# Kernel optimization log

Hardware: AMD Instinct MI355X
Metric: run time of the kernel (lower is better)

Reference implementation:

```python
import jax, jax.numpy as jnp
import numpy as np

EPS = 1e-5
LORA_DIM = 64
LORA_SCALE = LORA_DIM ** (-0.5)
GRAD_SCALE = 0.5  # infeat_grad_scale (bp_to_unet=True path)


def _ln(x, g=None, b=None):
    mu = jnp.mean(x, axis=-1, keepdims=True)
    var = jnp.mean((x - mu) ** 2, axis=-1, keepdims=True)
    y = (x - mu) * jax.lax.rsqrt(var + EPS)
    if g is not None:
        y = y * g + b
    return y


def _grad_scale(t, s=GRAD_SCALE):
    # identity in forward, scales gradient by s in backward
    return t * s + jax.lax.stop_gradient(t) * (1.0 - s)


def setup_inputs() -> dict:
    key = jax.random.key(0)
    ks = jax.random.split(key, 8)
    B, C, H, W = 32, 1280, 32, 32
    TD, LD = 768, LORA_DIM
    inp = {}
    inp["layer_infeat"] = jax.random.normal(ks[0], (B, C, H, W), jnp.float32)
    inp["layer_inquery"] = jax.random.normal(ks[1], (B, H * W, C), jnp.float32)
    inp["token_q_emb"] = jax.random.normal(ks[2], (TD,), jnp.float32)
    # learned params
    inp["to_q_w"] = jax.random.normal(ks[3], (C, TD), jnp.float32) * (TD ** -0.5)
    inp["ln_x_g"] = jnp.ones((C,), jnp.float32)
    inp["ln_x_b"] = jnp.zeros((C,), jnp.float32)
    inp["ln_k_g"] = jnp.ones((C,), jnp.float32)
    inp["ln_k_b"] = jnp.zeros((C,), jnp.float32)
    inp["ln_q_g"] = jnp.ones((TD,), jnp.float32)
    inp["ln_q_b"] = jnp.zeros((TD,), jnp.float32)
    inp["lora_q_w"] = jax.random.normal(ks[4], (LD, C), jnp.float32) * (C ** -0.5)
    inp["lora_k_w"] = jax.random.normal(ks[5], (LD, C), jnp.float32) * (C ** -0.5)
    inp["mask"] = jax.random.randint(ks[6], (B, 1, H, W), 0, 2).astype(jnp.float32)
    return inp


def reference(layer_infeat, layer_inquery, token_q_emb, to_q_w,
              ln_x_g, ln_x_b, ln_k_g, ln_k_b, ln_q_g, ln_q_b,
              lora_q_w, lora_k_w, mask):
    B, C, H, W = layer_infeat.shape
    # flatten(2).permute(0,2,1): [B,C,H,W] -> [B, HW, C]
    x = _grad_scale(layer_infeat).reshape(B, C, H * W).transpose(0, 2, 1)
    k_in = _grad_scale(layer_inquery)
    # q = to_q(ln_q(token_q_emb[None])) -> [1, C], broadcast to [B, 1, C]
    q = _ln(token_q_emb[None, :], ln_q_g, ln_q_b) @ to_q_w.T
    q = jnp.broadcast_to(q[None], (B, 1, C))
    k = _ln(k_in, ln_k_g, ln_k_b)   # [B, HW, C]
    v = _ln(x, ln_x_g, ln_x_b)      # [B, HW, C]
    # LoRA score path (use_lora=True since lora_dim>0)
    lora_q = _ln(q) @ lora_q_w.T    # [B, 1, LD]
    lora_k = _ln(k) @ lora_k_w.T    # [B, HW, LD]
    sim = jnp.einsum('bid,bjd->bij', lora_q, lora_k) * LORA_SCALE  # [B,1,HW]
    # mask: nearest interpolation to (H,W) is identity (same size); flatten
    m = mask.reshape(B, 1, H * W) > 0
    sim = jnp.where(m, sim, -jnp.finfo(sim.dtype).max)
    attn = jax.nn.softmax(sim, axis=-1)
    fg = jnp.einsum('bij,bjd->bid', attn, v)            # [B, 1, C]
    bg = jnp.mean(v, axis=1, keepdims=True) - fg        # [B, 1, C]
    out = jnp.concatenate([fg, bg], axis=-1)            # [B, 1, 2C]
    return out[:, 0, :]                                  # [B, 2C]
```

## Files before the change

kernel.cpp:

```cpp
#include <hip/hip_runtime.h>
#include <math.h>

#define B_   32
#define CD   1280
#define HW_  1024
#define TD_  768
#define LD_  64
#define EPSF 1e-5f
#define LORA_SCALE_F 0.125f

__device__ __forceinline__ float wredSum(float a) {
#pragma unroll
  for (int o = 32; o; o >>= 1) a += __shfl_xor(a, o, 64);
  return a;
}
__device__ __forceinline__ void wred2(float& a, float& b) {
#pragma unroll
  for (int o = 32; o; o >>= 1) { a += __shfl_xor(a, o, 64); b += __shfl_xor(b, o, 64); }
}
__device__ __forceinline__ float blockSum(float v, float* red) {
  int t = threadIdx.x;
  red[t] = v; __syncthreads();
#pragma unroll
  for (int s = 128; s > 0; s >>= 1) { if (t < s) red[t] += red[t + s]; __syncthreads(); }
  float r = red[0]; __syncthreads();
  return r;
}
__device__ __forceinline__ float blockMax(float v, float* red) {
  int t = threadIdx.x;
  red[t] = v; __syncthreads();
#pragma unroll
  for (int s = 128; s > 0; s >>= 1) { if (t < s) red[t] = fmaxf(red[t], red[t + s]); __syncthreads(); }
  float r = red[0]; __syncthreads();
  return r;
}
__device__ __forceinline__ void blockSum2(float& a, float& b, float2* red) {
  int t = threadIdx.x;
  red[t] = make_float2(a, b); __syncthreads();
#pragma unroll
  for (int s = 128; s > 0; s >>= 1) {
    if (t < s) { red[t].x += red[t + s].x; red[t].y += red[t + s].y; }
    __syncthreads();
  }
  a = red[0].x; b = red[0].y; __syncthreads();
}

__global__ __launch_bounds__(256) void kA12(const float* __restrict__ tq,
                                            const float* __restrict__ lng,
                                            const float* __restrict__ lnb,
                                            const float* __restrict__ to_q_w,
                                            float* __restrict__ q_out) {
  __shared__ float lnq[TD_];
  __shared__ float2 red[256];
  int t = threadIdx.x;
  float s = 0.f, ss = 0.f, vals[3];
#pragma unroll
  for (int k = 0; k < 3; k++) { float v = tq[t + 256 * k]; vals[k] = v; s += v; ss += v * v; }
  blockSum2(s, ss, red);
  float mu = s * (1.f / TD_);
  float r = rsqrtf(ss * (1.f / TD_) - mu * mu + EPSF);
#pragma unroll
  for (int k = 0; k < 3; k++) { int i = t + 256 * k; lnq[i] = (vals[k] - mu) * r * lng[i] + lnb[i]; }
  __syncthreads();
  int c = blockIdx.x * 4 + (t >> 6);
  int lane = t & 63;
  const float4* w4 = (const float4*)(to_q_w + (size_t)c * TD_);
  const float4* l4 = (const float4*)lnq;
  float dot = 0.f;
#pragma unroll
  for (int i = 0; i < 3; i++) {
    int f = i * 64 + lane;
    float4 w = w4[f], l = l4[f];
    dot += w.x * l.x + w.y * l.y + w.z * l.z + w.w * l.w;
  }
  dot = wredSum(dot);
  if (lane == 0) q_out[c] = dot;
}

__global__ __launch_bounds__(256) void kA34(const float* __restrict__ q_in,
                                            const float* __restrict__ lora_q_w,
                                            float* __restrict__ lq_out) {
  __shared__ float qs[CD];
  __shared__ float2 red[256];
  int t = threadIdx.x;
  float s = 0.f, ss = 0.f, vals[5];
#pragma unroll
  for (int k = 0; k < 5; k++) { float v = q_in[t + 256 * k]; vals[k] = v; s += v; ss += v * v; }
  blockSum2(s, ss, red);
  float mu = s * (1.f / CD);
  float r = rsqrtf(ss * (1.f / CD) - mu * mu + EPSF);
#pragma unroll
  for (int k = 0; k < 5; k++) { int i = t + 256 * k; qs[i] = (vals[k] - mu) * r; }
  __syncthreads();
  int d = blockIdx.x * 4 + (t >> 6);
  int lane = t & 63;
  const float4* w4 = (const float4*)(lora_q_w + (size_t)d * CD);
  const float4* q4 = (const float4*)qs;
  float dot = 0.f;
#pragma unroll
  for (int i = 0; i < 5; i++) {
    int f = i * 64 + lane;
    float4 w = w4[f], qq = q4[f];
    dot += w.x * qq.x + w.y * qq.y + w.z * qq.z + w.w * qq.w;
  }
  dot = wredSum(dot);
  if (lane == 0) lq_out[d] = dot;
}

__global__ __launch_bounds__(256) void kA56(const float* __restrict__ lq,
                                            const float* __restrict__ lora_k_w,
                                            float* __restrict__ w_eff) {
  __shared__ float l[LD_];
  int t = threadIdx.x;
  if (t < LD_) l[t] = lq[t];
  __syncthreads();
  int c = blockIdx.x * 256 + t;
  float acc = 0.f;
#pragma unroll 8
  for (int d = 0; d < LD_; d++) acc += l[d] * lora_k_w[(size_t)d * CD + c];
  w_eff[c] = acc;
}

__global__ __launch_bounds__(256) void kB(const float* __restrict__ kin,
                                          const float* __restrict__ g,
                                          const float* __restrict__ bb,
                                          const float* __restrict__ w_eff,
                                          float* __restrict__ sim) {
  __shared__ float4 gs[CD / 4], bs[CD / 4], ws[CD / 4];
  __shared__ float red[256];
  int t = threadIdx.x;
  float wsum = 0.f;
  for (int k = t; k < CD / 4; k += 256) {
    float4 w = ((const float4*)w_eff)[k];
    ws[k] = w;
    gs[k] = ((const float4*)g)[k];
    bs[k] = ((const float4*)bb)[k];
    wsum += w.x + w.y + w.z + w.w;
  }
  float W0 = blockSum(wsum, red);
  int wid = t >> 6, lane = t & 63;
  int gw = blockIdx.x * 4 + wid;
  for (int row = gw; row < B_ * HW_; row += 8192) {
    const float4* x4 = (const float4*)(kin + (size_t)row * CD);
    float4 xv[5];
    float s = 0.f, ss = 0.f;
#pragma unroll
    for (int i = 0; i < 5; i++) {
      float4 v = x4[i * 64 + lane];
      xv[i] = v;
      s += v.x + v.y + v.z + v.w;
      ss += v.x * v.x + v.y * v.y + v.z * v.z + v.w * v.w;
    }
    wred2(s, ss);
    float mu1 = s * (1.f / CD);
    float r1 = rsqrtf(ss * (1.f / CD) - mu1 * mu1 + EPSF);
    float s2 = 0.f, ss2 = 0.f;
#pragma unroll
    for (int i = 0; i < 5; i++) {
      int f = i * 64 + lane;
      float4 G = gs[f], Bv = bs[f], v = xv[i], kk;
      kk.x = (v.x - mu1) * r1 * G.x + Bv.x;
      kk.y = (v.y - mu1) * r1 * G.y + Bv.y;
      kk.z = (v.z - mu1) * r1 * G.z + Bv.z;
      kk.w = (v.w - mu1) * r1 * G.w + Bv.w;
      xv[i] = kk;
      s2 += kk.x + kk.y + kk.z + kk.w;
      ss2 += kk.x * kk.x + kk.y * kk.y + kk.z * kk.z + kk.w * kk.w;
    }
    wred2(s2, ss2);
    float mu2 = s2 * (1.f / CD);
    float r2 = rsqrtf(ss2 * (1.f / CD) - mu2 * mu2 + EPSF);
    float dot = 0.f;
#pragma unroll
    for (int i = 0; i < 5; i++) {
      float4 w = ws[i * 64 + lane], kk = xv[i];
      dot += w.x * kk.x + w.y * kk.y + w.z * kk.z + w.w * kk.w;
    }
    dot = wredSum(dot);
    if (lane == 0) sim[row] = LORA_SCALE_F * r2 * (dot - mu2 * W0);
  }
}

__global__ __launch_bounds__(256) void kD1(const float* __restrict__ infeat,
                                           float* __restrict__ mu_out,
                                           float* __restrict__ r_out) {
  int tile = blockIdx.x & 15, b = blockIdx.x >> 4;
  int t = threadIdx.x;
  int jg = t & 15;
  int slice = t >> 4;
  int j0 = tile * 64 + jg * 4;
  const float* base = infeat + (size_t)b * CD * HW_ + j0;
  float4 s = make_float4(0, 0, 0, 0), q = make_float4(0, 0, 0, 0);
  int c0 = slice * 80;
#pragma unroll 4
  for (int c = c0; c < c0 + 80; c++) {
    float4 v = *(const float4*)(base + (size_t)c * HW_);
    s.x += v.x; s.y += v.y; s.z += v.z; s.w += v.w;
    q.x += v.x * v.x; q.y += v.y * v.y; q.z += v.z * v.z; q.w += v.w * v.w;
  }
  __shared__ float4 sArr[16][16], qArr[16][16];
  sArr[slice][jg] = s; qArr[slice][jg] = q;
  __syncthreads();
#pragma unroll
  for (int st = 8; st > 0; st >>= 1) {
    if (slice < st) {
      float4 a = sArr[slice][jg], b2 = sArr[slice + st][jg];
      a.x += b2.x; a.y += b2.y; a.z += b2.z; a.w += b2.w;
      sArr[slice][jg] = a;
      a = qArr[slice][jg]; b2 = qArr[slice + st][jg];
      a.x += b2.x; a.y += b2.y; a.z += b2.z; a.w += b2.w;
      qArr[slice][jg] = a;
    }
    __syncthreads();
  }
  if (slice == 0) {
    float4 S = sArr[0][jg], Q = qArr[0][jg], mu, r;
    mu.x = S.x * (1.f / CD); mu.y = S.y * (1.f / CD);
    mu.z = S.z * (1.f / CD); mu.w = S.w * (1.f / CD);
    r.x = rsqrtf(Q.x * (1.f / CD) - mu.x * mu.x + EPSF);
    r.y = rsqrtf(Q.y * (1.f / CD) - mu.y * mu.y + EPSF);
    r.z = rsqrtf(Q.z * (1.f / CD) - mu.z * mu.z + EPSF);
    r.w = rsqrtf(Q.w * (1.f / CD) - mu.w * mu.w + EPSF);
    int j = b * HW_ + j0;
    *(float4*)(mu_out + j) = mu;
    *(float4*)(r_out + j) = r;
  }
}

__global__ __launch_bounds__(256) void kC(const float* __restrict__ sim,
                                          const float* __restrict__ mask,
                                          const float* __restrict__ mu,
                                          const float* __restrict__ r,
                                          float* __restrict__ w1,
                                          float* __restrict__ w2,
                                          float* __restrict__ S1,
                                          float* __restrict__ S3) {
  __shared__ float red[256];
  __shared__ float2 red2[256];
  int b = blockIdx.x, t = threadIdx.x;
  float4 sv = ((const float4*)(sim + b * HW_))[t];
  float4 mv = ((const float4*)(mask + b * HW_))[t];
  float4 muv = ((const float4*)(mu + b * HW_))[t];
  float4 rv = ((const float4*)(r + b * HW_))[t];
  const float NEG = -3.4028235e38f;
  float se0 = mv.x > 0.f ? sv.x : NEG;
  float se1 = mv.y > 0.f ? sv.y : NEG;
  float se2 = mv.z > 0.f ? sv.z : NEG;
  float se3 = mv.w > 0.f ? sv.w : NEG;
  float m = fmaxf(fmaxf(se0, se1), fmaxf(se2, se3));
  float M = blockMax(m, red);
  float e0 = expf(se0 - M), e1 = expf(se1 - M), e2 = expf(se2 - M), e3 = expf(se3 - M);
  float Z = blockSum(e0 + e1 + e2 + e3, red);
  float inv = 1.f / Z;
  float a0 = e0 * inv, a1 = e1 * inv, a2 = e2 * inv, a3 = e3 * inv;
  float4 w1v = make_float4(a0 * rv.x, a1 * rv.y, a2 * rv.z, a3 * rv.w);
  float4 w2v = make_float4(rv.x * (1.f / HW_), rv.y * (1.f / HW_),
                           rv.z * (1.f / HW_), rv.w * (1.f / HW_));
  float s1 = w1v.x * muv.x + w1v.y * muv.y + w1v.z * muv.z + w1v.w * muv.w;
  float s3 = w2v.x * muv.x + w2v.y * muv.y + w2v.z * muv.z + w2v.w * muv.w;
  blockSum2(s1, s3, red2);
  ((float4*)(w1 + b * HW_))[t] = w1v;
  ((float4*)(w2 + b * HW_))[t] = w2v;
  if (t == 0) { S1[b] = s1; S3[b] = s3; }
}

__global__ __launch_bounds__(256) void kD2(const float* __restrict__ infeat,
                                           const float* __restrict__ w1,
                                           const float* __restrict__ w2,
                                           const float* __restrict__ S1,
                                           const float* __restrict__ S3,
                                           const float* __restrict__ g,
                                           const float* __restrict__ bb,
                                           float* __restrict__ out) {
  __shared__ float4 w1s[HW_ / 4], w2s[HW_ / 4];
  int t = threadIdx.x;
  int b = blockIdx.x / 40, tile = blockIdx.x % 40;
  w1s[t] = ((const float4*)(w1 + b * HW_))[t];
  w2s[t] = ((const float4*)(w2 + b * HW_))[t];
  __syncthreads();
  int wid = t >> 6, lane = t & 63;
  float s1 = S1[b], s3 = S3[b];
#pragma unroll
  for (int k = 0; k < 8; k++) {
    int c = tile * 32 + wid * 8 + k;
    const float4* x4 = (const float4*)(infeat + (size_t)b * CD * HW_ + (size_t)c * HW_);
    float d1 = 0.f, d2 = 0.f;
#pragma unroll
    for (int i = 0; i < 4; i++) {
      int f = i * 64 + lane;
      float4 x = x4[f], a = w1s[f], w = w2s[f];
      d1 += x.x * a.x + x.y * a.y + x.z * a.z + x.w * a.w;
      d2 += x.x * w.x + x.y * w.y + x.z * w.z + x.w * w.w;
    }
    wred2(d1, d2);
    if (lane == 0) {
      float gc = g[c], bc = bb[c];
      float fg = gc * (d1 - s1) + bc;
      float vm = gc * (d2 - s3) + bc;
      out[(size_t)b * (2 * CD) + c] = fg;
      out[(size_t)b * (2 * CD) + CD + c] = vm - fg;
    }
  }
}

extern "C" void kernel_launch(void* const* d_in, const int* in_sizes, int n_in,
                              void* d_out, int out_size, void* d_ws, size_t ws_size,
                              hipStream_t stream) {
  const float* infeat  = (const float*)d_in[0];
  const float* inquery = (const float*)d_in[1];
  const float* tq      = (const float*)d_in[2];
  const float* to_q_w  = (const float*)d_in[3];
  const float* ln_x_g  = (const float*)d_in[4];
  const float* ln_x_b  = (const float*)d_in[5];
  const float* ln_k_g  = (const float*)d_in[6];
  const float* ln_k_b  = (const float*)d_in[7];
  const float* ln_q_g  = (const float*)d_in[8];
  const float* ln_q_b  = (const float*)d_in[9];
  const float* lora_q_w = (const float*)d_in[10];
  const float* lora_k_w = (const float*)d_in[11];
  const float* mask    = (const float*)d_in[12];
  float* out = (float*)d_out;

  float* ws = (float*)d_ws;
  float* q_ws    = ws;
  float* lq_ws   = ws + 1280;
  float* weff_ws = ws + 1344;
  float* sim_ws  = ws + 2624;
  float* mu_ws   = ws + 35392;
  float* r_ws    = ws + 68160;
  float* w1_ws   = ws + 100928;
  float* w2_ws   = ws + 133696;
  float* S1_ws   = ws + 166464;
  float* S3_ws   = ws + 166496;

  kA12<<<320, 256, 0, stream>>>(tq, ln_q_g, ln_q_b, to_q_w, q_ws);
  kA34<<<16, 256, 0, stream>>>(q_ws, lora_q_w, lq_ws);
  kA56<<<5, 256, 0, stream>>>(lq_ws, lora_k_w, weff_ws);
  kB<<<2048, 256, 0, stream>>>(inquery, ln_k_g, ln_k_b, weff_ws, sim_ws);
  kD1<<<512, 256, 0, stream>>>(infeat, mu_ws, r_ws);
  kC<<<32, 256, 0, stream>>>(sim_ws, mask, mu_ws, r_ws, w1_ws, w2_ws, S1_ws, S3_ws);
  kD2<<<1280, 256, 0, stream>>>(infeat, w1_ws, w2_ws, S1_ws, S3_ws, ln_x_g, ln_x_b, out);
}
```

Baseline: 405.6 us.

## Fuse kernels, compute LN-of-LN scores via moment algebra, split infeat stats

Merges the query projection with the infeat channel-statistics pass into one launch, and folds the LoRA q/k weight prep into a single-block prep kernel. The prep kernel emits per-channel coefficients and global scalars so the key-row kernel computes the double layernorm and score from one pass of moment sums, without materialising normalised values. The infeat stats pass is split into four channel quarters for more blocks, and the softmax/weight kernel is fused into the final reduction, which now recomputes mu/r and softmax in every tile block. This cuts launches and per-row work at the cost of redundant softmax work, extra shuffles and a single-block serial prep step. The one-pass variance expansion may also lose some numerical precision.

```diff
diff --git a/kernel.cpp b/kernel.cpp
--- a/kernel.cpp
+++ b/kernel.cpp
@@ -8,6 +8,7 @@
 #define LD_  64
 #define EPSF 1e-5f
 #define LORA_SCALE_F 0.125f
+#define NROWS (B_ * HW_)
 
 __device__ __forceinline__ float wredSum(float a) {
 #pragma unroll
@@ -45,241 +46,276 @@
   a = red[0].x; b = red[0].y; __syncthreads();
 }
 
-__global__ __launch_bounds__(256) void kA12(const float* __restrict__ tq,
+__global__ __launch_bounds__(256) void kAD1(const float* __restrict__ tq,
                                             const float* __restrict__ lng,
                                             const float* __restrict__ lnb,
                                             const float* __restrict__ to_q_w,
-                                            float* __restrict__ q_out) {
-  __shared__ float lnq[TD_];
-  __shared__ float2 red[256];
-  int t = threadIdx.x;
-  float s = 0.f, ss = 0.f, vals[3];
-#pragma unroll
-  for (int k = 0; k < 3; k++) { float v = tq[t + 256 * k]; vals[k] = v; s += v; ss += v * v; }
-  blockSum2(s, ss, red);
-  float mu = s * (1.f / TD_);
-  float r = rsqrtf(ss * (1.f / TD_) - mu * mu + EPSF);
-#pragma unroll
-  for (int k = 0; k < 3; k++) { int i = t + 256 * k; lnq[i] = (vals[k] - mu) * r * lng[i] + lnb[i]; }
-  __syncthreads();
-  int c = blockIdx.x * 4 + (t >> 6);
-  int lane = t & 63;
-  const float4* w4 = (const float4*)(to_q_w + (size_t)c * TD_);
-  const float4* l4 = (const float4*)lnq;
-  float dot = 0.f;
-#pragma unroll
-  for (int i = 0; i < 3; i++) {
-    int f = i * 64 + lane;
-    float4 w = w4[f], l = l4[f];
-    dot += w.x * l.x + w.y * l.y + w.z * l.z + w.w * l.w;
-  }
-  dot = wredSum(dot);
-  if (lane == 0) q_out[c] = dot;
-}
-
-__global__ __launch_bounds__(256) void kA34(const float* __restrict__ q_in,
-                                            const float* __restrict__ lora_q_w,
-                                            float* __restrict__ lq_out) {
-  __shared__ float qs[CD];
-  __shared__ float2 red[256];
-  int t = threadIdx.x;
-  float s = 0.f, ss = 0.f, vals[5];
-#pragma unroll
-  for (int k = 0; k < 5; k++) { float v = q_in[t + 256 * k]; vals[k] = v; s += v; ss += v * v; }
-  blockSum2(s, ss, red);
-  float mu = s * (1.f / CD);
-  float r = rsqrtf(ss * (1.f / CD) - mu * mu + EPSF);
-#pragma unroll
-  for (int k = 0; k < 5; k++) { int i = t + 256 * k; qs[i] = (vals[k] - mu) * r; }
-  __syncthreads();
-  int d = blockIdx.x * 4 + (t >> 6);
-  int lane = t & 63;
-  const float4* w4 = (const float4*)(lora_q_w + (size_t)d * CD);
-  const float4* q4 = (const float4*)qs;
-  float dot = 0.f;
+                                            const float* __restrict__ infeat,
+                                            float* __restrict__ q_out,
+                                            float* __restrict__ Spart,
+                                            float* __restrict__ Qpart) {
+  __shared__ float smem[2048];
+  int t = threadIdx.x;
+  if (blockIdx.x < 320) {
+    float* lnq = smem;
+    float2* red = (float2*)(smem + 768);
+    float s = 0.f, ss = 0.f, vals[3];
+#pragma unroll
+    for (int k = 0; k < 3; k++) { float v = tq[t + 256 * k]; vals[k] = v; s += v; ss += v * v; }
+    blockSum2(s, ss, red);
+    float mu = s * (1.f / TD_);
+    float r = rsqrtf(ss * (1.f / TD_) - mu * mu + EPSF);
+#pragma unroll
+    for (int k = 0; k < 3; k++) { int i = t + 256 * k; lnq[i] = (vals[k] - mu) * r * lng[i] + lnb[i]; }
+    __syncthreads();
+    int c = blockIdx.x * 4 + (t >> 6);
+    int lane = t & 63;
+    const float4* w4 = (const float4*)(to_q_w + (size_t)c * TD_);
+    const float4* l4 = (const float4*)lnq;
+    float dot = 0.f;
+#pragma unroll
+    for (int i = 0; i < 3; i++) {
+      int f = i * 64 + lane;
+      float4 w = w4[f], l = l4[f];
+      dot += w.x * l.x + w.y * l.y + w.z * l.z + w.w * l.w;
+    }
+    dot = wredSum(dot);
+    if (lane == 0) q_out[c] = dot;
+  } else {
+    int idx = blockIdx.x - 320;
+    int b = idx >> 6;
+    int rr = idx & 63;
+    int tile = rr >> 2;
+    int qtr = rr & 3;
+    int jg = t & 15;
+    int slice = t >> 4;
+    int j0 = tile * 64 + jg * 4;
+    const float* base = infeat + (size_t)b * CD * HW_ + j0;
+    int c0 = qtr * 320 + slice * 20;
+    float4 s = make_float4(0, 0, 0, 0), q = make_float4(0, 0, 0, 0);
+#pragma unroll
+    for (int c = c0; c < c0 + 20; c++) {
+      float4 v = *(const float4*)(base + (size_t)c * HW_);
+      s.x += v.x; s.y += v.y; s.z += v.z; s.w += v.w;
+      q.x += v.x * v.x; q.y += v.y * v.y; q.z += v.z * v.z; q.w += v.w * v.w;
+    }
+    float4* sArr = (float4*)smem;
+    float4* qArr = (float4*)(smem + 1024);
+    sArr[slice * 16 + jg] = s; qArr[slice * 16 + jg] = q;
+    __syncthreads();
+#pragma unroll
+    for (int st = 8; st > 0; st >>= 1) {
+      if (slice < st) {
+        float4 a = sArr[slice * 16 + jg], b2 = sArr[(slice + st) * 16 + jg];
+        a.x += b2.x; a.y += b2.y; a.z += b2.z; a.w += b2.w;
+        sArr[slice * 16 + jg] = a;
+        a = qArr[slice * 16 + jg]; b2 = qArr[(slice + st) * 16 + jg];
+        a.x += b2.x; a.y += b2.y; a.z += b2.z; a.w += b2.w;
+        qArr[slice * 16 + jg] = a;
+      }
+      __syncthreads();
+    }
+    if (slice == 0) {
+      size_t o = ((size_t)(b * 4 + qtr) << 10) + j0;
+      *(float4*)(Spart + o) = sArr[jg];
+      *(float4*)(Qpart + o) = qArr[jg];
+    }
+  }
+}
+
+__global__ __launch_bounds__(1024) void kPrep(const float* __restrict__ q_in,
+                                              const float* __restrict__ lora_q_w,
+                                              const float* __restrict__ lora_k_w,
+                                              const float* __restrict__ kg,
+                                              const float* __restrict__ kb,
+                                              float4* __restrict__ coeff,
+                                              float* __restrict__ scalars) {
+  __shared__ float qn[CD];
+  __shared__ float lqs[LD_];
+  __shared__ float4 red4[1024];
+  int t = threadIdx.x;
+  float v0 = q_in[t];
+  float v1 = (t < CD - 1024) ? q_in[1024 + t] : 0.f;
+  red4[t] = make_float4(v0 + v1, v0 * v0 + v1 * v1, 0.f, 0.f);
+  __syncthreads();
+#pragma unroll
+  for (int st = 512; st > 0; st >>= 1) {
+    if (t < st) { red4[t].x += red4[t + st].x; red4[t].y += red4[t + st].y; }
+    __syncthreads();
+  }
+  float mu = red4[0].x * (1.f / CD);
+  float r = rsqrtf(red4[0].y * (1.f / CD) - mu * mu + EPSF);
+  __syncthreads();
+  qn[t] = (v0 - mu) * r;
+  if (t < CD - 1024) qn[1024 + t] = (v1 - mu) * r;
+  __syncthreads();
+  int w = t >> 6, lane = t & 63;
+  int d0 = w * 4;
+  const float4* qn4 = (const float4*)qn;
+  float dacc[4] = {0.f, 0.f, 0.f, 0.f};
 #pragma unroll
   for (int i = 0; i < 5; i++) {
     int f = i * 64 + lane;
-    float4 w = w4[f], qq = q4[f];
-    dot += w.x * qq.x + w.y * qq.y + w.z * qq.z + w.w * qq.w;
-  }
-  dot = wredSum(dot);
-  if (lane == 0) lq_out[d] = dot;
-}
-
-__global__ __launch_bounds__(256) void kA56(const float* __restrict__ lq,
-                                            const float* __restrict__ lora_k_w,
-                                            float* __restrict__ w_eff) {
-  __shared__ float l[LD_];
-  int t = threadIdx.x;
-  if (t < LD_) l[t] = lq[t];
-  __syncthreads();
-  int c = blockIdx.x * 256 + t;
-  float acc = 0.f;
-#pragma unroll 8
-  for (int d = 0; d < LD_; d++) acc += l[d] * lora_k_w[(size_t)d * CD + c];
-  w_eff[c] = acc;
+    float4 qv = qn4[f];
+#pragma unroll
+    for (int dd = 0; dd < 4; dd++) {
+      float4 wv = *(const float4*)(lora_q_w + (size_t)(d0 + dd) * CD + 4 * f);
+      dacc[dd] += wv.x * qv.x + wv.y * qv.y + wv.z * qv.z + wv.w * qv.w;
+    }
+  }
+#pragma unroll
+  for (int o = 32; o; o >>= 1) {
+#pragma unroll
+    for (int dd = 0; dd < 4; dd++) dacc[dd] += __shfl_xor(dacc[dd], o, 64);
+  }
+  if (lane == 0) {
+#pragma unroll
+    for (int dd = 0; dd < 4; dd++) lqs[d0 + dd] = dacc[dd];
+  }
+  __syncthreads();
+  float4 pA = make_float4(0, 0, 0, 0);
+  float4 pB = make_float4(0, 0, 0, 0);
+#pragma unroll
+  for (int pass = 0; pass < 2; pass++) {
+    int c = (pass == 0) ? t : 1024 + t;
+    if (pass == 0 || t < CD - 1024) {
+      float acc = 0.f;
+#pragma unroll 16
+      for (int d = 0; d < LD_; d++) acc += lqs[d] * lora_k_w[(size_t)d * CD + c];
+      float g = kg[c], b = kb[c], wv = acc;
+      coeff[c] = make_float4(g * g, g * b, wv * g, g);
+      pA.x += g; pA.y += g * g; pA.z += g * b; pA.w += b;
+      pB.x += b * b; pB.y += wv * g; pB.z += wv * b; pB.w += wv;
+    }
+  }
+  red4[t] = pA; __syncthreads();
+#pragma unroll
+  for (int st = 512; st > 0; st >>= 1) {
+    if (t < st) {
+      red4[t].x += red4[t + st].x; red4[t].y += red4[t + st].y;
+      red4[t].z += red4[t + st].z; red4[t].w += red4[t + st].w;
+    }
+    __syncthreads();
+  }
+  if (t == 0) {
+    scalars[0] = red4[0].x; scalars[1] = red4[0].y;
+    scalars[2] = red4[0].z; scalars[3] = red4[0].w;
+  }
+  __syncthreads();
+  red4[t] = pB; __syncthreads();
+#pragma unroll
+  for (int st = 512; st > 0; st >>= 1) {
+    if (t < st) {
+      red4[t].x += red4[t + st].x; red4[t].y += red4[t + st].y;
+      red4[t].z += red4[t + st].z; red4[t].w += red4[t + st].w;
+    }
+    __syncthreads();
+  }
+  if (t == 0) {
+    scalars[4] = red4[0].x; scalars[5] = red4[0].y;
+    scalars[6] = red4[0].z; scalars[7] = red4[0].w;
+  }
 }
 
 __global__ __launch_bounds__(256) void kB(const float* __restrict__ kin,
-                                          const float* __restrict__ g,
-                                          const float* __restrict__ bb,
-                                          const float* __restrict__ w_eff,
+                                          const float4* __restrict__ coeff,
+                                          const float* __restrict__ scalars,
                                           float* __restrict__ sim) {
-  __shared__ float4 gs[CD / 4], bs[CD / 4], ws[CD / 4];
-  __shared__ float red[256];
-  int t = threadIdx.x;
-  float wsum = 0.f;
-  for (int k = t; k < CD / 4; k += 256) {
-    float4 w = ((const float4*)w_eff)[k];
-    ws[k] = w;
-    gs[k] = ((const float4*)g)[k];
-    bs[k] = ((const float4*)bb)[k];
-    wsum += w.x + w.y + w.z + w.w;
-  }
-  float W0 = blockSum(wsum, red);
-  int wid = t >> 6, lane = t & 63;
-  int gw = blockIdx.x * 4 + wid;
-  for (int row = gw; row < B_ * HW_; row += 8192) {
+  int t = threadIdx.x, wid = t >> 6, lane = t & 63;
+  float4 cf[20];
+#pragma unroll
+  for (int i = 0; i < 5; i++) {
+    int f = i * 64 + lane;
+#pragma unroll
+    for (int k = 0; k < 4; k++) cf[i * 4 + k] = coeff[f * 4 + k];
+  }
+  float Sg = scalars[0], Sg2 = scalars[1], Sgb = scalars[2], Sb = scalars[3];
+  float Sb2 = scalars[4], Swg = scalars[5], Swb = scalars[6], W0 = scalars[7];
+  int row0 = blockIdx.x * 4 + wid;
+  for (int row = row0; row < NROWS; row += 8192) {
     const float4* x4 = (const float4*)(kin + (size_t)row * CD);
-    float4 xv[5];
-    float s = 0.f, ss = 0.f;
+    float sx = 0.f, sxx = 0.f, sA = 0.f, sB = 0.f, sC = 0.f, sD = 0.f, sE = 0.f;
 #pragma unroll
     for (int i = 0; i < 5; i++) {
       float4 v = x4[i * 64 + lane];
-      xv[i] = v;
-      s += v.x + v.y + v.z + v.w;
-      ss += v.x * v.x + v.y * v.y + v.z * v.z + v.w * v.w;
-    }
-    wred2(s, ss);
-    float mu1 = s * (1.f / CD);
-    float r1 = rsqrtf(ss * (1.f / CD) - mu1 * mu1 + EPSF);
-    float s2 = 0.f, ss2 = 0.f;
-#pragma unroll
-    for (int i = 0; i < 5; i++) {
-      int f = i * 64 + lane;
-      float4 G = gs[f], Bv = bs[f], v = xv[i], kk;
-      kk.x = (v.x - mu1) * r1 * G.x + Bv.x;
-      kk.y = (v.y - mu1) * r1 * G.y + Bv.y;
-      kk.z = (v.z - mu1) * r1 * G.z + Bv.z;
-      kk.w = (v.w - mu1) * r1 * G.w + Bv.w;
-      xv[i] = kk;
-      s2 += kk.x + kk.y + kk.z + kk.w;
-      ss2 += kk.x * kk.x + kk.y * kk.y + kk.z * kk.z + kk.w * kk.w;
-    }
-    wred2(s2, ss2);
-    float mu2 = s2 * (1.f / CD);
-    float r2 = rsqrtf(ss2 * (1.f / CD) - mu2 * mu2 + EPSF);
-    float dot = 0.f;
-#pragma unroll
-    for (int i = 0; i < 5; i++) {
-      float4 w = ws[i * 64 + lane], kk = xv[i];
-      dot += w.x * kk.x + w.y * kk.y + w.z * kk.z + w.w * kk.w;
-    }
-    dot = wredSum(dot);
-    if (lane == 0) sim[row] = LORA_SCALE_F * r2 * (dot - mu2 * W0);
-  }
-}
-
-__global__ __launch_bounds__(256) void kD1(const float* __restrict__ infeat,
-                                           float* __restrict__ mu_out,
-                                           float* __restrict__ r_out) {
-  int tile = blockIdx.x & 15, b = blockIdx.x >> 4;
-  int t = threadIdx.x;
-  int jg = t & 15;
-  int slice = t >> 4;
-  int j0 = tile * 64 + jg * 4;
-  const float* base = infeat + (size_t)b * CD * HW_ + j0;
-  float4 s = make_float4(0, 0, 0, 0), q = make_float4(0, 0, 0, 0);
-  int c0 = slice * 80;
-#pragma unroll 4
-  for (int c = c0; c < c0 + 80; c++) {
-    float4 v = *(const float4*)(base + (size_t)c * HW_);
-    s.x += v.x; s.y += v.y; s.z += v.z; s.w += v.w;
-    q.x += v.x * v.x; q.y += v.y * v.y; q.z += v.z * v.z; q.w += v.w * v.w;
-  }
-  __shared__ float4 sArr[16][16], qArr[16][16];
-  sArr[slice][jg] = s; qArr[slice][jg] = q;
-  __syncthreads();
-#pragma unroll
-  for (int st = 8; st > 0; st >>= 1) {
-    if (slice < st) {
-      float4 a = sArr[slice][jg], b2 = sArr[slice + st][jg];
-      a.x += b2.x; a.y += b2.y; a.z += b2.z; a.w += b2.w;
-      sArr[slice][jg] = a;
-      a = qArr[slice][jg]; b2 = qArr[slice + st][jg];
-      a.x += b2.x; a.y += b2.y; a.z += b2.z; a.w += b2.w;
-      qArr[slice][jg] = a;
-    }
-    __syncthreads();
-  }
-  if (slice == 0) {
-    float4 S = sArr[0][jg], Q = qArr[0][jg], mu, r;
-    mu.x = S.x * (1.f / CD); mu.y = S.y * (1.f / CD);
-    mu.z = S.z * (1.f / CD); mu.w = S.w * (1.f / CD);
-    r.x = rsqrtf(Q.x * (1.f / CD) - mu.x * mu.x + EPSF);
-    r.y = rsqrtf(Q.y * (1.f / CD) - mu.y * mu.y + EPSF);
-    r.z = rsqrtf(Q.z * (1.f / CD) - mu.z * mu.z + EPSF);
-    r.w = rsqrtf(Q.w * (1.f / CD) - mu.w * mu.w + EPSF);
-    int j = b * HW_ + j0;
-    *(float4*)(mu_out + j) = mu;
-    *(float4*)(r_out + j) = r;
-  }
-}
-
-__global__ __launch_bounds__(256) void kC(const float* __restrict__ sim,
-                                          const float* __restrict__ mask,
-                                          const float* __restrict__ mu,
-                                          const float* __restrict__ r,
-                                          float* __restrict__ w1,
-                                          float* __restrict__ w2,
-                                          float* __restrict__ S1,
-                                          float* __restrict__ S3) {
+      float xs[4] = {v.x, v.y, v.z, v.w};
+#pragma unroll
+      for (int k = 0; k < 4; k++) {
+        float x = xs[k];
+        float4 c = cf[i * 4 + k];
+        float xx = x * x;
+        sx += x; sxx += xx;
+        sA += c.x * xx; sB += c.x * x; sC += c.y * x; sD += c.z * x; sE += c.w * x;
+      }
+    }
+#pragma unroll
+    for (int o = 32; o; o >>= 1) {
+      sx += __shfl_xor(sx, o, 64);  sxx += __shfl_xor(sxx, o, 64);
+      sA += __shfl_xor(sA, o, 64);  sB += __shfl_xor(sB, o, 64);
+      sC += __shfl_xor(sC, o, 64);  sD += __shfl_xor(sD, o, 64);
+      sE += __shfl_xor(sE, o, 64);
+    }
+    float mu1 = sx * (1.f / CD);
+    float r1 = rsqrtf(sxx * (1.f / CD) - mu1 * mu1 + EPSF);
+    float Sk = r1 * (sE - mu1 * Sg) + Sb;
+    float Sk2 = r1 * r1 * (sA - 2.f * mu1 * sB + mu1 * mu1 * Sg2)
+              + 2.f * r1 * (sC - mu1 * Sgb) + Sb2;
+    float Swk = r1 * (sD - mu1 * Swg) + Swb;
+    float mu2 = Sk * (1.f / CD);
+    float r2 = rsqrtf(Sk2 * (1.f / CD) - mu2 * mu2 + EPSF);
+    if (lane == 0) sim[row] = LORA_SCALE_F * r2 * (Swk - mu2 * W0);
+  }
+}
+
+__global__ __launch_bounds__(256) void kCD2(const float* __restrict__ infeat,
+                                            const float* __restrict__ sim,
+                                            const float* __restrict__ mask,
+                                            const float* __restrict__ Spart,
+                                            const float* __restrict__ Qpart,
+                                            const float* __restrict__ g,
+                                            const float* __restrict__ bb,
+                                            float* __restrict__ out) {
+  __shared__ float4 w1s[HW_ / 4], w2s[HW_ / 4];
   __shared__ float red[256];
   __shared__ float2 red2[256];
-  int b = blockIdx.x, t = threadIdx.x;
+  int t = threadIdx.x;
+  int b = blockIdx.x / 40, tile = blockIdx.x % 40;
+  float4 S = make_float4(0, 0, 0, 0), Q = make_float4(0, 0, 0, 0);
+#pragma unroll
+  for (int q = 0; q < 4; q++) {
+    size_t o = ((size_t)(b * 4 + q) << 10);
+    float4 sp = ((const float4*)(Spart + o))[t];
+    float4 qp = ((const float4*)(Qpart + o))[t];
+    S.x += sp.x; S.y += sp.y; S.z += sp.z; S.w += sp.w;
+    Q.x += qp.x; Q.y += qp.y; Q.z += qp.z; Q.w += qp.w;
+  }
+  float4 muv, rv;
+  muv.x = S.x * (1.f / CD); muv.y = S.y * (1.f / CD);
+  muv.z = S.z * (1.f / CD); muv.w = S.w * (1.f / CD);
+  rv.x = rsqrtf(Q.x * (1.f / CD) - muv.x * muv.x + EPSF);
+  rv.y = rsqrtf(Q.y * (1.f / CD) - muv.y * muv.y + EPSF);
+  rv.z = rsqrtf(Q.z * (1.f / CD) - muv.z * muv.z + EPSF);
+  rv.w = rsqrtf(Q.w * (1.f / CD) - muv.w * muv.w + EPSF);
   float4 sv = ((const float4*)(sim + b * HW_))[t];
   float4 mv = ((const float4*)(mask + b * HW_))[t];
-  float4 muv = ((const float4*)(mu + b * HW_))[t];
-  float4 rv = ((const float4*)(r + b * HW_))[t];
   const float NEG = -3.4028235e38f;
   float se0 = mv.x > 0.f ? sv.x : NEG;
   float se1 = mv.y > 0.f ? sv.y : NEG;
   float se2 = mv.z > 0.f ? sv.z : NEG;
   float se3 = mv.w > 0.f ? sv.w : NEG;
-  float m = fmaxf(fmaxf(se0, se1), fmaxf(se2, se3));
-  float M = blockMax(m, red);
+  float M = blockMax(fmaxf(fmaxf(se0, se1), fmaxf(se2, se3)), red);
   float e0 = expf(se0 - M), e1 = expf(se1 - M), e2 = expf(se2 - M), e3 = expf(se3 - M);
   float Z = blockSum(e0 + e1 + e2 + e3, red);
   float inv = 1.f / Z;
-  float a0 = e0 * inv, a1 = e1 * inv, a2 = e2 * inv, a3 = e3 * inv;
-  float4 w1v = make_float4(a0 * rv.x, a1 * rv.y, a2 * rv.z, a3 * rv.w);
+  float4 w1v = make_float4(e0 * inv * rv.x, e1 * inv * rv.y, e2 * inv * rv.z, e3 * inv * rv.w);
   float4 w2v = make_float4(rv.x * (1.f / HW_), rv.y * (1.f / HW_),
                            rv.z * (1.f / HW_), rv.w * (1.f / HW_));
   float s1 = w1v.x * muv.x + w1v.y * muv.y + w1v.z * muv.z + w1v.w * muv.w;
   float s3 = w2v.x * muv.x + w2v.y * muv.y + w2v.z * muv.z + w2v.w * muv.w;
   blockSum2(s1, s3, red2);
-  ((float4*)(w1 + b * HW_))[t] = w1v;
-  ((float4*)(w2 + b * HW_))[t] = w2v;
-  if (t == 0) { S1[b] = s1; S3[b] = s3; }
-}
-
-__global__ __launch_bounds__(256) void kD2(const float* __restrict__ infeat,
-                                           const float* __restrict__ w1,
-                                           const float* __restrict__ w2,
-                                           const float* __restrict__ S1,
-                                           const float* __restrict__ S3,
-                                           const float* __restrict__ g,
-                                           const float* __restrict__ bb,
-                                           float* __restrict__ out) {
-  __shared__ float4 w1s[HW_ / 4], w2s[HW_ / 4];
-  int t = threadIdx.x;
-  int b = blockIdx.x / 40, tile = blockIdx.x % 40;
-  w1s[t] = ((const float4*)(w1 + b * HW_))[t];
-  w2s[t] = ((const float4*)(w2 + b * HW_))[t];
+  w1s[t] = w1v; w2s[t] = w2v;
   __syncthreads();
   int wid = t >> 6, lane = t & 63;
-  float s1 = S1[b], s3 = S3[b];
 #pragma unroll
   for (int k = 0; k < 8; k++) {
     int c = tile * 32 + wid * 8 + k;
@@ -322,22 +358,18 @@
   float* out = (float*)d_out;
 
   float* ws = (float*)d_ws;
-  float* q_ws    = ws;
-  float* lq_ws   = ws + 1280;
-  float* weff_ws = ws + 1344;
-  float* sim_ws  = ws + 2624;
-  float* mu_ws   = ws + 35392;
-  float* r_ws    = ws + 68160;
-  float* w1_ws   = ws + 100928;
-  float* w2_ws   = ws + 133696;
-  float* S1_ws   = ws + 166464;
-  float* S3_ws   = ws + 166496;
-
-  kA12<<<320, 256, 0, stream>>>(tq, ln_q_g, ln_q_b, to_q_w, q_ws);
-  kA34<<<16, 256, 0, stream>>>(q_ws, lora_q_w, lq_ws);
-  kA56<<<5, 256, 0, stream>>>(lq_ws, lora_k_w, weff_ws);
-  kB<<<2048, 256, 0, stream>>>(inquery, ln_k_g, ln_k_b, weff_ws, sim_ws);
-  kD1<<<512, 256, 0, stream>>>(infeat, mu_ws, r_ws);
-  kC<<<32, 256, 0, stream>>>(sim_ws, mask, mu_ws, r_ws, w1_ws, w2_ws, S1_ws, S3_ws);
-  kD2<<<1280, 256, 0, stream>>>(infeat, w1_ws, w2_ws, S1_ws, S3_ws, ln_x_g, ln_x_b, out);
-}
+  float* q_ws      = ws;
+  float* coeff_ws  = ws + 1280;
+  float* scal_ws   = ws + 6400;
+  float* sim_ws    = ws + 6408;
+  float* Spart_ws  = ws + 39176;
+  float* Qpart_ws  = ws + 170248;
+
+  kAD1<<<2368, 256, 0, stream>>>(tq, ln_q_g, ln_q_b, to_q_w, infeat,
+                                 q_ws, Spart_ws, Qpart_ws);
+  kPrep<<<1, 1024, 0, stream>>>(q_ws, lora_q_w, lora_k_w, ln_k_g, ln_k_b,
+                                (float4*)coeff_ws, scal_ws);
+  kB<<<2048, 256, 0, stream>>>(inquery, (const float4*)coeff_ws, scal_ws, sim_ws);
+  kCD2<<<1280, 256, 0, stream>>>(infeat, sim_ws, mask, Spart_ws, Qpart_ws,
+                                 ln_x_g, ln_x_b, out);
+}
```

Result: slower. 414.3 us (+2.1%).
